# Kernel tuning notes

Measured on AMD Instinct MI355X. Metric: run time of the kernel, lower is better.

## Reference

```python
import jax, jax.numpy as jnp
from jax import lax
import numpy as np

B, L, F = 4, 1024, 32
DM, NL, DS, DC, EX, NH = 256, 4, 16, 4, 2, 4
DI = EX * DM            # 512 inner channels
DTR = (DM + 15) // 16   # dt_rank = 16


def setup_inputs() -> dict:
    key = jax.random.key(0)
    ks = jax.random.split(key, 12)
    s = 0.02
    rn = lambda k, shape: jax.random.normal(k, shape, jnp.float32) * s
    return dict(
        x=jax.random.normal(ks[0], (B, L, F), jnp.float32),
        proj_w=rn(ks[1], (DM, F)), proj_b=jnp.zeros((DM,), jnp.float32),
        inproj_w=rn(ks[2], (NL, 2 * DI, DM)),
        conv_w=rn(ks[3], (NL, DI, DC)), conv_b=jnp.zeros((NL, DI), jnp.float32),
        xproj_w=rn(ks[4], (NL, DTR + 2 * DS, DI)),
        dtproj_w=rn(ks[5], (NL, DI, DTR)), dtproj_b=rn(ks[6], (NL, DI)),
        A_log=jnp.tile(jnp.log(jnp.arange(1, DS + 1, dtype=jnp.float32))[None, None, :], (NL, DI, 1)),
        Dp=jnp.ones((NL, DI), jnp.float32),
        outproj_w=rn(ks[7], (NL, DM, DI)),
        ln_g=jnp.ones((NL, DM), jnp.float32), ln_b=jnp.zeros((NL, DM), jnp.float32),
        head_w1=rn(ks[8], (DM, DM)), head_b1=jnp.zeros((DM,), jnp.float32),
        head_w2=rn(ks[9], (NH, DM)), head_b2=jnp.zeros((NH,), jnp.float32),
    )


def _layernorm(x, g, b, eps=1e-5):
    mu = x.mean(axis=-1, keepdims=True)
    var = ((x - mu) ** 2).mean(axis=-1, keepdims=True)
    return (x - mu) * lax.rsqrt(var + eps) * g + b


def _mamba(x, inw, cw, cb, xpw, dtw, dtb, A_log, Dp, outw):
    b, l, _ = x.shape
    xz = x @ inw.T                       # (b,l,2*DI)
    u, z = xz[..., :DI], xz[..., DI:]
    # causal depthwise conv1d, kernel DC
    up = jnp.pad(u, ((0, 0), (DC - 1, 0), (0, 0)))
    uc = sum(up[:, k:k + l, :] * cw[:, k] for k in range(DC)) + cb
    uc = jax.nn.silu(uc)
    dbc = uc @ xpw.T                     # (b,l,DTR+2*DS)
    dt, Bc, Cc = dbc[..., :DTR], dbc[..., DTR:DTR + DS], dbc[..., DTR + DS:]
    delta = jax.nn.softplus(dt @ dtw.T + dtb)   # (b,l,DI)
    A = -jnp.exp(A_log)                  # (DI,DS)

    def step(h, inp):
        d_t, B_t, C_t, u_t = inp         # (b,DI),(b,DS),(b,DS),(b,DI)
        h = jnp.exp(d_t[..., None] * A) * h + (d_t * u_t)[..., None] * B_t[:, None, :]
        return h, jnp.einsum('bdn,bn->bd', h, C_t)

    h0 = jnp.zeros((b, DI, DS), x.dtype)
    xs = tuple(jnp.swapaxes(a, 0, 1) for a in (delta, Bc, Cc, uc))
    _, ys = lax.scan(step, h0, xs)       # ys: (l,b,DI)
    y = jnp.swapaxes(ys, 0, 1) + uc * Dp
    return (y * jax.nn.silu(z)) @ outw.T


def reference(x, proj_w, proj_b, inproj_w, conv_w, conv_b, xproj_w, dtproj_w, dtproj_b,
              A_log, Dp, outproj_w, ln_g, ln_b, head_w1, head_b1, head_w2, head_b2):
    h = x @ proj_w.T + proj_b
    for i in range(NL):
        blk = _mamba(h, inproj_w[i], conv_w[i], conv_b[i], xproj_w[i],
                     dtproj_w[i], dtproj_b[i], A_log[i], Dp[i], outproj_w[i])
        h = h + _layernorm(blk, ln_g[i], ln_b[i])
    p = h.mean(axis=1)                   # (b,DM) pool over time
    hid = jax.nn.relu(p @ head_w1.T + head_b1)
    return hid @ head_w2.T + head_b2     # (b,NH)
```

## Files before the change

kernel.cpp:

```cpp
#include <hip/hip_runtime.h>
#include <hip/hip_fp16.h>
#include <math.h>

#define LTOT 1024
#define BB   4
#define F_IN 32
#define DM   256
#define DI   512
#define DS   16
#define DTRN 16
#define NXP  48
#define NLAY 4
#define NH   4
#define NC   16
#define CLEN 64
#define ROWS (BB*LTOT)

typedef _Float16 half8 __attribute__((ext_vector_type(8)));
typedef float f32x16 __attribute__((ext_vector_type(16)));
typedef unsigned short us8 __attribute__((ext_vector_type(8)));

__device__ __forceinline__ float siluf_(float x) { return x / (1.0f + expf(-x)); }
__device__ __forceinline__ float softplusf_(float x) {
    if (x > 20.f) return x;
    if (x < -20.f) return expf(x);
    return log1pf(expf(x));
}

__device__ __forceinline__ void split16(float x, unsigned short& hi, unsigned short& lo) {
    __half h = __float2half(x);
    hi = *(unsigned short*)&h;
    float r = x - __half2float(h);
    __half l = __float2half(r);
    lo = *(unsigned short*)&l;
}

__global__ __launch_bounds__(256) void k_splitw(const float* __restrict__ inw,
                                                const float* __restrict__ outw,
                                                unsigned short* __restrict__ iwh,
                                                unsigned short* __restrict__ iwl,
                                                unsigned short* __restrict__ owh,
                                                unsigned short* __restrict__ owl) {
    int q = blockIdx.x * 256 + threadIdx.x;
    ushort4 h4, l4;
    if (q < 262144) {
        float4 v = ((const float4*)inw)[q];
        split16(v.x, h4.x, l4.x); split16(v.y, h4.y, l4.y);
        split16(v.z, h4.z, l4.z); split16(v.w, h4.w, l4.w);
        *(ushort4*)(iwh + (size_t)q * 4) = h4;
        *(ushort4*)(iwl + (size_t)q * 4) = l4;
    } else {
        int r = q - 262144;
        float4 v = ((const float4*)outw)[r];
        split16(v.x, h4.x, l4.x); split16(v.y, h4.y, l4.y);
        split16(v.z, h4.z, l4.z); split16(v.w, h4.w, l4.w);
        *(ushort4*)(owh + (size_t)r * 4) = h4;
        *(ushort4*)(owl + (size_t)r * 4) = l4;
    }
}

__global__ __launch_bounds__(256) void k_proj(const float* __restrict__ x,
                                              const float* __restrict__ pw,
                                              const float* __restrict__ pb,
                                              float* __restrict__ h,
                                              unsigned short* __restrict__ hh,
                                              unsigned short* __restrict__ hl) {
    __shared__ float wl[DM][33];
    __shared__ float xl[16][32];
    int t = threadIdx.x;
    int r0 = blockIdx.x * 16;
    for (int i = t; i < DM * 32 / 4; i += 256) {
        float4 v = ((const float4*)pw)[i];
        int c = i / 8, k = (i % 8) * 4;
        wl[c][k] = v.x; wl[c][k + 1] = v.y; wl[c][k + 2] = v.z; wl[c][k + 3] = v.w;
    }
    for (int i = t; i < 16 * 32 / 4; i += 256) {
        float4 v = ((const float4*)(x + (size_t)r0 * F_IN))[i];
        int r = i / 8, k = (i % 8) * 4;
        xl[r][k] = v.x; xl[r][k + 1] = v.y; xl[r][k + 2] = v.z; xl[r][k + 3] = v.w;
    }
    __syncthreads();
    int c = t;
    float bias = pb[c];
    float acc[16];
#pragma unroll
    for (int r = 0; r < 16; ++r) acc[r] = bias;
    for (int k = 0; k < 32; ++k) {
        float w = wl[c][k];
#pragma unroll
        for (int r = 0; r < 16; ++r) acc[r] = fmaf(xl[r][k], w, acc[r]);
    }
#pragma unroll
    for (int r = 0; r < 16; ++r) {
        size_t idx = (size_t)(r0 + r) * DM + c;
        h[idx] = acc[r];
        unsigned short vh, vl; split16(acc[r], vh, vl);
        hh[idx] = vh; hl[idx] = vl;
    }
}

__global__ __launch_bounds__(256) void k_gemm_xz(const unsigned short* __restrict__ Ahp,
                                                 const unsigned short* __restrict__ Alp,
                                                 const unsigned short* __restrict__ Bhp,
                                                 const unsigned short* __restrict__ Blp,
                                                 float* __restrict__ C) {
    __shared__ unsigned short Ah[64][40], Al[64][40], Bh[128][40], Bl[128][40];
    int t = threadIdx.x;
    int bx = blockIdx.x & 7;
    int by = blockIdx.x >> 3;
    int rowA = t >> 2, kA = (t & 3) * 8;
    int rowB = t >> 1, kB = (t & 1) * 16;
    const unsigned short* ApH = Ahp + (size_t)(by * 64 + rowA) * DM + kA;
    const unsigned short* ApL = Alp + (size_t)(by * 64 + rowA) * DM + kA;
    const unsigned short* BpH = Bhp + (size_t)(bx * 128 + rowB) * DM + kB;
    const unsigned short* BpL = Blp + (size_t)(bx * 128 + rowB) * DM + kB;
    us8 rah = *(const us8*)ApH, ral = *(const us8*)ApL;
    us8 rbh0 = *(const us8*)BpH, rbh1 = *(const us8*)(BpH + 8);
    us8 rbl0 = *(const us8*)BpL, rbl1 = *(const us8*)(BpL + 8);
    int lane = t & 63, wid = t >> 6;
    int fr = lane & 31, fg = lane >> 5;
    int wr = wid >> 1, wc = wid & 1;
    f32x16 acc[2] = {};
    for (int k0 = 0; k0 < DM; k0 += 32) {
        *(us8*)&Ah[rowA][kA] = rah;
        *(us8*)&Al[rowA][kA] = ral;
        *(us8*)&Bh[rowB][kB] = rbh0; *(us8*)&Bh[rowB][kB + 8] = rbh1;
        *(us8*)&Bl[rowB][kB] = rbl0; *(us8*)&Bl[rowB][kB + 8] = rbl1;
        __syncthreads();
        if (k0 + 32 < DM) {
            rah = *(const us8*)(ApH + k0 + 32); ral = *(const us8*)(ApL + k0 + 32);
            rbh0 = *(const us8*)(BpH + k0 + 32); rbh1 = *(const us8*)(BpH + k0 + 40);
            rbl0 = *(const us8*)(BpL + k0 + 32); rbl1 = *(const us8*)(BpL + k0 + 40);
        }
#pragma unroll
        for (int s = 0; s < 2; ++s) {
            int ko = s * 16 + fg * 8;
            half8 ah = *(const half8*)&Ah[wr * 32 + fr][ko];
            half8 al = *(const half8*)&Al[wr * 32 + fr][ko];
#pragma unroll
            for (int fc = 0; fc < 2; ++fc) {
                half8 bh = *(const half8*)&Bh[wc * 64 + fc * 32 + fr][ko];
                half8 bl = *(const half8*)&Bl[wc * 64 + fc * 32 + fr][ko];
                acc[fc] = __builtin_amdgcn_mfma_f32_32x32x16_f16(ah, bh, acc[fc], 0, 0, 0);
                acc[fc] = __builtin_amdgcn_mfma_f32_32x32x16_f16(ah, bl, acc[fc], 0, 0, 0);
                acc[fc] = __builtin_amdgcn_mfma_f32_32x32x16_f16(al, bh, acc[fc], 0, 0, 0);
            }
        }
        __syncthreads();
    }
    float* Cp = C + (size_t)(by * 64 + wr * 32) * 1024 + bx * 128 + wc * 64;
#pragma unroll
    for (int fc = 0; fc < 2; ++fc) {
#pragma unroll
        for (int reg = 0; reg < 16; ++reg) {
            int row = (reg & 3) + 8 * (reg >> 2) + 4 * fg;
            Cp[(size_t)row * 1024 + fc * 32 + fr] = acc[fc][reg];
        }
    }
}

__global__ __launch_bounds__(256) void k_conv(const float* __restrict__ xz,
                                              const float* __restrict__ cw,
                                              const float* __restrict__ cb,
                                              float* __restrict__ uc) {
    int gid = blockIdx.x * 256 + threadIdx.x;
    if (gid >= ROWS * (DI / 4)) return;
    int r = gid / (DI / 4);
    int d = (gid % (DI / 4)) * 4;
    int tt = r & (LTOT - 1);
    float4 acc = make_float4(cb[d], cb[d + 1], cb[d + 2], cb[d + 3]);
#pragma unroll
    for (int k = 0; k < 4; ++k) {
        int ts = tt - 3 + k;
        if (ts < 0) continue;
        float4 u = *(const float4*)(xz + (size_t)(r - 3 + k) * 1024 + d);
        acc.x = fmaf(u.x, cw[(d + 0) * 4 + k], acc.x);
        acc.y = fmaf(u.y, cw[(d + 1) * 4 + k], acc.y);
        acc.z = fmaf(u.z, cw[(d + 2) * 4 + k], acc.z);
        acc.w = fmaf(u.w, cw[(d + 3) * 4 + k], acc.w);
    }
    acc.x = siluf_(acc.x); acc.y = siluf_(acc.y); acc.z = siluf_(acc.z); acc.w = siluf_(acc.w);
    *(float4*)(uc + (size_t)r * DI + d) = acc;
}

__global__ __launch_bounds__(256) void k_dbcp(const float* __restrict__ uc,
                                              const float* __restrict__ xpw,
                                              float* __restrict__ xz) {
    __shared__ float us[32][132];
    __shared__ float wsd[48][132];
    int t = threadIdx.x;
    int kp = blockIdx.x & 3;
    int r0 = (blockIdx.x >> 2) * 32;
    int k0 = kp * 128;
    float4* us4 = (float4*)us;
    float4* ws4 = (float4*)wsd;
#pragma unroll
    for (int j = 0; j < 4; ++j) {
        int i = t + j * 256;
        int r = i >> 5, kq = i & 31;
        us4[r * 33 + kq] = *(const float4*)(uc + (size_t)(r0 + r) * DI + k0 + kq * 4);
    }
#pragma unroll
    for (int j = 0; j < 6; ++j) {
        int i = t + j * 256;
        int r = i >> 5, kq = i & 31;
        ws4[r * 33 + kq] = *(const float4*)(xpw + (size_t)r * DI + k0 + kq * 4);
    }
    __syncthreads();
    int tx = t & 15, ty = t >> 4;
    const float4* ua = us4 + (ty * 2) * 33;
    const float4* ub = ua + 33;
    const float4* w0p = ws4 + (tx * 3) * 33;
    const float4* w1p = w0p + 33;
    const float4* w2p = w0p + 66;
    float acc[2][3] = {};
#pragma unroll 4
    for (int kq = 0; kq < 32; ++kq) {
        float4 u0 = ua[kq], u1 = ub[kq];
        float4 w0 = w0p[kq], w1 = w1p[kq], w2 = w2p[kq];
        acc[0][0] = fmaf(u0.x, w0.x, acc[0][0]); acc[0][0] = fmaf(u0.y, w0.y, acc[0][0]);
        acc[0][0] = fmaf(u0.z, w0.z, acc[0][0]); acc[0][0] = fmaf(u0.w, w0.w, acc[0][0]);
        acc[0][1] = fmaf(u0.x, w1.x, acc[0][1]); acc[0][1] = fmaf(u0.y, w1.y, acc[0][1]);
        acc[0][1] = fmaf(u0.z, w1.z, acc[0][1]); acc[0][1] = fmaf(u0.w, w1.w, acc[0][1]);
        acc[0][2] = fmaf(u0.x, w2.x, acc[0][2]); acc[0][2] = fmaf(u0.y, w2.y, acc[0][2]);
        acc[0][2] = fmaf(u0.z, w2.z, acc[0][2]); acc[0][2] = fmaf(u0.w, w2.w, acc[0][2]);
        acc[1][0] = fmaf(u1.x, w0.x, acc[1][0]); acc[1][0] = fmaf(u1.y, w0.y, acc[1][0]);
        acc[1][0] = fmaf(u1.z, w0.z, acc[1][0]); acc[1][0] = fmaf(u1.w, w0.w, acc[1][0]);
        acc[1][1] = fmaf(u1.x, w1.x, acc[1][1]); acc[1][1] = fmaf(u1.y, w1.y, acc[1][1]);
        acc[1][1] = fmaf(u1.z, w1.z, acc[1][1]); acc[1][1] = fmaf(u1.w, w1.w, acc[1][1]);
        acc[1][2] = fmaf(u1.x, w2.x, acc[1][2]); acc[1][2] = fmaf(u1.y, w2.y, acc[1][2]);
        acc[1][2] = fmaf(u1.z, w2.z, acc[1][2]); acc[1][2] = fmaf(u1.w, w2.w, acc[1][2]);
    }
    float* outp = xz + (size_t)(r0 + ty * 2) * 1024 + kp * 48 + tx * 3;
    outp[0] = acc[0][0]; outp[1] = acc[0][1]; outp[2] = acc[0][2];
    outp[1024] = acc[1][0]; outp[1025] = acc[1][1]; outp[1026] = acc[1][2];
}

__global__ __launch_bounds__(256) void k_dbcr(const float* __restrict__ xzp,
                                              const float* __restrict__ dtw,
                                              const float* __restrict__ dtb,
                                              float* __restrict__ delta,
                                              float* __restrict__ BC) {
    __shared__ float dbl[16][NXP];
    int t = threadIdx.x;
    int r0 = blockIdx.x * 16;
    {
        int r = t >> 4, c3 = (t & 15) * 3;
        const float* pp = xzp + (size_t)(r0 + r) * 1024 + c3;
#pragma unroll
        for (int j = 0; j < 3; ++j) {
            float s = pp[j] + pp[48 + j] + pp[96 + j] + pp[144 + j];
            dbl[r][c3 + j] = s;
            int cj = c3 + j;
            if (cj >= 16) BC[(size_t)(r0 + r) * 32 + (cj - 16)] = s;
        }
    }
    __syncthreads();
    {
        int c0 = t * 2;
        float wd0[16], wd1[16];
        const float4* q0 = (const float4*)(dtw + (size_t)c0 * 16);
        const float4* q1 = (const float4*)(dtw + (size_t)(c0 + 1) * 16);
#pragma unroll
        for (int j = 0; j < 4; ++j) { *(float4*)&wd0[j * 4] = q0[j]; *(float4*)&wd1[j * 4] = q1[j]; }
        float bb0 = dtb[c0], bb1 = dtb[c0 + 1];
        for (int r = 0; r < 16; ++r) {
            float s0 = bb0, s1 = bb1;
#pragma unroll
            for (int k = 0; k < 16; ++k) {
                float dv = dbl[r][k];
                s0 = fmaf(dv, wd0[k], s0);
                s1 = fmaf(dv, wd1[k], s1);
            }
            *(float2*)(delta + (size_t)(r0 + r) * DI + c0) =
                make_float2(softplusf_(s0), softplusf_(s1));
        }
    }
}

__global__ __launch_bounds__(256) void k_scanA(const float* __restrict__ delta,
                                               const float* __restrict__ uc,
                                               const float* __restrict__ BC,
                                               const float* __restrict__ A_log,
                                               float* __restrict__ P,
                                               float* __restrict__ hL) {
    __shared__ float2 du2[CLEN][16];
    __shared__ float  Bl[CLEN][16];
    int bid = blockIdx.x;
    int c = bid & 15, dblk = (bid >> 4) & 31, b = bid >> 9;
    int d0 = dblk * 16, t0 = c * CLEN;
    int t = threadIdx.x;
    {
        int row = t >> 2, hf = (t & 3) * 4;
        size_t rbase = (size_t)(b * LTOT + t0 + row);
        float4 dv = *(const float4*)(delta + rbase * DI + d0 + hf);
        float4 uv = *(const float4*)(uc + rbase * DI + d0 + hf);
        float4* dst = (float4*)&du2[row][hf];
        dst[0] = make_float4(dv.x, uv.x, dv.y, uv.y);
        dst[1] = make_float4(dv.z, uv.z, dv.w, uv.w);
        *(float4*)&Bl[row][hf] = *(const float4*)(BC + rbase * 32 + hf);
    }
    __syncthreads();
    int n = t & 15, dn = t >> 4;
    float Ac = -expf(A_log[(size_t)(d0 + dn) * DS + n]);
    float h = 0.f, Pp = 1.f;
#pragma unroll 8
    for (int k = 0; k < CLEN; ++k) {
        float2 du = du2[k][dn];
        float Bv = Bl[k][n];
        float a = expf(du.x * Ac);
        Pp *= a;
        h = fmaf(a, h, du.x * du.y * Bv);
    }
    size_t idx = ((size_t)(b * NC + c)) * (DI * DS) + (size_t)d0 * DS + t;
    P[idx] = Pp;
    hL[idx] = h;
}

__global__ __launch_bounds__(256) void k_scanC(const float* __restrict__ delta,
                                               const float* __restrict__ uc,
                                               const float* __restrict__ BC,
                                               const float* __restrict__ A_log,
                                               const float* __restrict__ P,
                                               const float* __restrict__ hL,
                                               const float* __restrict__ Dp,
                                               const float* __restrict__ xz,
                                               unsigned short* __restrict__ yh,
                                               unsigned short* __restrict__ yl) {
    __shared__ float2 du2[CLEN][16];
    __shared__ float2 bc2[CLEN][16];
    __shared__ float  ytmp[16][16][20];
    int bid = blockIdx.x;
    int c = bid & 15, dblk = (bid >> 4) & 31, b = bid >> 9;
    int d0 = dblk * 16, t0 = c * CLEN;
    int t = threadIdx.x;
    {
        int row = t >> 2, hf = (t & 3) * 4;
        size_t rbase = (size_t)(b * LTOT + t0 + row);
        float4 dv = *(const float4*)(delta + rbase * DI + d0 + hf);
        float4 uv = *(const float4*)(uc + rbase * DI + d0 + hf);
        float4* dst = (float4*)&du2[row][hf];
        dst[0] = make_float4(dv.x, uv.x, dv.y, uv.y);
        dst[1] = make_float4(dv.z, uv.z, dv.w, uv.w);
        float4 bv = *(const float4*)(BC + rbase * 32 + hf);
        float4 cv = *(const float4*)(BC + rbase * 32 + 16 + hf);
        float4* bdst = (float4*)&bc2[row][hf];
        bdst[0] = make_float4(bv.x, cv.x, bv.y, cv.y);
        bdst[1] = make_float4(bv.z, cv.z, bv.w, cv.w);
    }
    __syncthreads();
    int n = t & 15, dn = t >> 4;
    float Ac = -expf(A_log[(size_t)(d0 + dn) * DS + n]);
    float Hin = 0.f;
    for (int cc = 0; cc < c; ++cc) {
        size_t idx = ((size_t)(b * NC + cc)) * (DI * DS) + (size_t)d0 * DS + t;
        Hin = fmaf(P[idx], Hin, hL[idx]);
    }
    float h = Hin;
    int rdn = t & 15, rk = t >> 4;
    float DpV = Dp[d0 + rdn];
    for (int s = 0; s < CLEN / 16; ++s) {
#pragma unroll
        for (int kk = 0; kk < 16; ++kk) {
            int k = s * 16 + kk;
            float2 du = du2[k][dn];
            float2 bc = bc2[k][n];
            float a = expf(du.x * Ac);
            h = fmaf(a, h, du.x * du.y * bc.x);
            ytmp[kk][dn][n] = h * bc.y;
        }
        __syncthreads();
        {
            const float* rowp = &ytmp[rk][rdn][0];
            float4 v0 = *(const float4*)(rowp + 0);
            float4 v1 = *(const float4*)(rowp + 4);
            float4 v2 = *(const float4*)(rowp + 8);
            float4 v3 = *(const float4*)(rowp + 12);
            float y = ((v0.x + v0.y) + (v0.z + v0.w)) + ((v1.x + v1.y) + (v1.z + v1.w))
                    + ((v2.x + v2.y) + (v2.z + v2.w)) + ((v3.x + v3.y) + (v3.z + v3.w));
            float uu = du2[s * 16 + rk][rdn].y;
            size_t rb2 = (size_t)(b * LTOT + t0 + s * 16 + rk);
            float z = xz[rb2 * 1024 + 512 + d0 + rdn];
            float val = fmaf(uu, DpV, y) * siluf_(z);
            unsigned short vh, vl; split16(val, vh, vl);
            size_t yi = rb2 * DI + d0 + rdn;
            yh[yi] = vh; yl[yi] = vl;
        }
        __syncthreads();
    }
}

__global__ __launch_bounds__(256) void k_gemm_out(const unsigned short* __restrict__ Ahp,
                                                  const unsigned short* __restrict__ Alp,
                                                  const unsigned short* __restrict__ Bhp,
                                                  const unsigned short* __restrict__ Blp,
                                                  float* __restrict__ p01,
                                                  float* __restrict__ p23) {
    __shared__ unsigned short Ah[64][40], Al[64][40], Bh[128][40], Bl[128][40];
    int t = threadIdx.x;
    int bx = blockIdx.x & 1;
    int by = (blockIdx.x >> 1) & 63;
    int kp = blockIdx.x >> 7;
    int rowA = t >> 2, kA = (t & 3) * 8;
    int rowB = t >> 1, kB = (t & 1) * 16;
    const unsigned short* ApH = Ahp + (size_t)(by * 64 + rowA) * DI + kp * 128 + kA;
    const unsigned short* ApL = Alp + (size_t)(by * 64 + rowA) * DI + kp * 128 + kA;
    const unsigned short* BpH = Bhp + (size_t)(bx * 128 + rowB) * DI + kp * 128 + kB;
    const unsigned short* BpL = Blp + (size_t)(bx * 128 + rowB) * DI + kp * 128 + kB;
    us8 rah = *(const us8*)ApH, ral = *(const us8*)ApL;
    us8 rbh0 = *(const us8*)BpH, rbh1 = *(const us8*)(BpH + 8);
    us8 rbl0 = *(const us8*)BpL, rbl1 = *(const us8*)(BpL + 8);
    int lane = t & 63, wid = t >> 6;
    int fr = lane & 31, fg = lane >> 5;
    int wr = wid >> 1, wc = wid & 1;
    f32x16 acc[2] = {};
    for (int k0 = 0; k0 < 128; k0 += 32) {
        *(us8*)&Ah[rowA][kA] = rah;
        *(us8*)&Al[rowA][kA] = ral;
        *(us8*)&Bh[rowB][kB] = rbh0; *(us8*)&Bh[rowB][kB + 8] = rbh1;
        *(us8*)&Bl[rowB][kB] = rbl0; *(us8*)&Bl[rowB][kB + 8] = rbl1;
        __syncthreads();
        if (k0 + 32 < 128) {
            rah = *(const us8*)(ApH + k0 + 32); ral = *(const us8*)(ApL + k0 + 32);
            rbh0 = *(const us8*)(BpH + k0 + 32); rbh1 = *(const us8*)(BpH + k0 + 40);
            rbl0 = *(const us8*)(BpL + k0 + 32); rbl1 = *(const us8*)(BpL + k0 + 40);
        }
#pragma unroll
        for (int s = 0; s < 2; ++s) {
            int ko = s * 16 + fg * 8;
            half8 ah = *(const half8*)&Ah[wr * 32 + fr][ko];
            half8 al = *(const half8*)&Al[wr * 32 + fr][ko];
#pragma unroll
            for (int fc = 0; fc < 2; ++fc) {
                half8 bh = *(const half8*)&Bh[wc * 64 + fc * 32 + fr][ko];
                half8 bl = *(const half8*)&Bl[wc * 64 + fc * 32 + fr][ko];
                acc[fc] = __builtin_amdgcn_mfma_f32_32x32x16_f16(ah, bh, acc[fc], 0, 0, 0);
                acc[fc] = __builtin_amdgcn_mfma_f32_32x32x16_f16(ah, bl, acc[fc], 0, 0, 0);
                acc[fc] = __builtin_amdgcn_mfma_f32_32x32x16_f16(al, bh, acc[fc], 0, 0, 0);
            }
        }
        __syncthreads();
    }
    float* pbase = (kp < 2 ? p01 : p23) + (size_t)(kp & 1) * (ROWS * DM);
    float* Cp = pbase + (size_t)(by * 64 + wr * 32) * DM + bx * 128 + wc * 64;
#pragma unroll
    for (int fc = 0; fc < 2; ++fc) {
#pragma unroll
        for (int reg = 0; reg < 16; ++reg) {
            int row = (reg & 3) + 8 * (reg >> 2) + 4 * fg;
            Cp[(size_t)row * DM + fc * 32 + fr] = acc[fc][reg];
        }
    }
}

__global__ __launch_bounds__(256) void k_ln_res(const float* __restrict__ p01,
                                                const float* __restrict__ p23,
                                                const float* __restrict__ g,
                                                const float* __restrict__ bb,
                                                float* __restrict__ h,
                                                unsigned short* __restrict__ hh,
                                                unsigned short* __restrict__ hl) {
    __shared__ float scratch[4];
    int r = blockIdx.x, t = threadIdx.x;
    size_t idx = (size_t)r * DM + t;
    float v = p01[idx] + p01[idx + (size_t)ROWS * DM] + p23[idx] + p23[idx + (size_t)ROWS * DM];
    float s = v;
#pragma unroll
    for (int m = 32; m >= 1; m >>= 1) s += __shfl_xor(s, m, 64);
    if ((t & 63) == 0) scratch[t >> 6] = s;
    __syncthreads();
    float mu = (scratch[0] + scratch[1] + scratch[2] + scratch[3]) * (1.f / DM);
    __syncthreads();
    float d = v - mu;
    float s2 = d * d;
#pragma unroll
    for (int m = 32; m >= 1; m >>= 1) s2 += __shfl_xor(s2, m, 64);
    if ((t & 63) == 0) scratch[t >> 6] = s2;
    __syncthreads();
    float var = (scratch[0] + scratch[1] + scratch[2] + scratch[3]) * (1.f / DM);
    float rstd = 1.f / sqrtf(var + 1e-5f);
    float nv = h[idx] + d * rstd * g[t] + bb[t];
    h[idx] = nv;
    unsigned short vh, vl; split16(nv, vh, vl);
    hh[idx] = vh; hl[idx] = vl;
}

__global__ __launch_bounds__(256) void k_meanp(const float* __restrict__ h,
                                               float* __restrict__ part) {
    int bid = blockIdx.x;
    int b = bid >> 3, g = bid & 7;
    int t = threadIdx.x;
    float s = 0.f;
    for (int k = 0; k < 128; ++k)
        s += h[(size_t)(b * LTOT + g * 128 + k) * DM + t];
    part[(size_t)bid * DM + t] = s;
}

__global__ __launch_bounds__(256) void k_head(const float* __restrict__ part,
                                              const float* __restrict__ w1,
                                              const float* __restrict__ b1,
                                              const float* __restrict__ w2,
                                              const float* __restrict__ b2,
                                              float* __restrict__ out) {
    __shared__ float pl[DM], hl[DM];
    int b = blockIdx.x, t = threadIdx.x;
    float s = 0.f;
    for (int g = 0; g < 8; ++g) s += part[(size_t)(b * 8 + g) * DM + t];
    pl[t] = s * (1.f / LTOT);
    __syncthreads();
    float a = b1[t];
    for (int k = 0; k < DM; ++k) a = fmaf(pl[k], w1[(size_t)t * DM + k], a);
    hl[t] = fmaxf(a, 0.f);
    __syncthreads();
    if (t < NH) {
        float o = b2[t];
        for (int k = 0; k < DM; ++k) o = fmaf(hl[k], w2[(size_t)t * DM + k], o);
        out[b * NH + t] = o;
    }
}

extern "C" void kernel_launch(void* const* d_in, const int* in_sizes, int n_in,
                              void* d_out, int out_size, void* d_ws, size_t ws_size,
                              hipStream_t stream) {
    const float* x        = (const float*)d_in[0];
    const float* proj_w   = (const float*)d_in[1];
    const float* proj_b   = (const float*)d_in[2];
    const float* inproj_w = (const float*)d_in[3];
    const float* conv_w   = (const float*)d_in[4];
    const float* conv_b   = (const float*)d_in[5];
    const float* xproj_w  = (const float*)d_in[6];
    const float* dtproj_w = (const float*)d_in[7];
    const float* dtproj_b = (const float*)d_in[8];
    const float* A_log    = (const float*)d_in[9];
    const float* Dp       = (const float*)d_in[10];
    const float* outproj_w= (const float*)d_in[11];
    const float* ln_g     = (const float*)d_in[12];
    const float* ln_b     = (const float*)d_in[13];
    const float* head_w1  = (const float*)d_in[14];
    const float* head_b1  = (const float*)d_in[15];
    const float* head_w2  = (const float*)d_in[16];
    const float* head_b2  = (const float*)d_in[17];

    float* ws    = (float*)d_ws;
    float* h     = ws;
    float* xz    = h + 1048576;
    float* uc    = xz + 4194304;
    float* delta = uc + 2097152;
    float* BC    = delta + 2097152;
    float* Pbuf  = BC + 131072;
    float* hLbuf = Pbuf + 524288;
    float* part  = hLbuf + 524288;
    unsigned short* h_hi  = (unsigned short*)(part + 8192);
    unsigned short* h_lo  = h_hi + 1048576;
    unsigned short* y_hi  = h_lo + 1048576;
    unsigned short* y_lo  = y_hi + 2097152;
    unsigned short* iw_hi = y_lo + 2097152;
    unsigned short* iw_lo = iw_hi + 1048576;
    unsigned short* ow_hi = iw_lo + 1048576;
    unsigned short* ow_lo = ow_hi + 524288;

    k_splitw<<<1536, 256, 0, stream>>>(inproj_w, outproj_w, iw_hi, iw_lo, ow_hi, ow_lo);
    k_proj<<<ROWS / 16, 256, 0, stream>>>(x, proj_w, proj_b, h, h_hi, h_lo);

    for (int i = 0; i < NLAY; ++i) {
        const float* cwi  = conv_w + (size_t)i * DI * 4;
        const float* cbi  = conv_b + (size_t)i * DI;
        const float* xpw  = xproj_w + (size_t)i * NXP * DI;
        const float* dtw  = dtproj_w + (size_t)i * DI * DTRN;
        const float* dtb  = dtproj_b + (size_t)i * DI;
        const float* Ali  = A_log + (size_t)i * DI * DS;
        const float* Dpi  = Dp + (size_t)i * DI;
        const float* gi   = ln_g + (size_t)i * DM;
        const float* bi   = ln_b + (size_t)i * DM;

        k_gemm_xz<<<512, 256, 0, stream>>>(h_hi, h_lo,
                                           iw_hi + (size_t)i * 262144, iw_lo + (size_t)i * 262144, xz);
        k_conv<<<ROWS * (DI / 4) / 256, 256, 0, stream>>>(xz, cwi, cbi, uc);
        k_dbcp<<<512, 256, 0, stream>>>(uc, xpw, xz);
        k_dbcr<<<ROWS / 16, 256, 0, stream>>>(xz, dtw, dtb, delta, BC);
        k_scanA<<<BB * 32 * NC, 256, 0, stream>>>(delta, uc, BC, Ali, Pbuf, hLbuf);
        k_scanC<<<BB * 32 * NC, 256, 0, stream>>>(delta, uc, BC, Ali, Pbuf, hLbuf, Dpi, xz, y_hi, y_lo);
        k_gemm_out<<<512, 256, 0, stream>>>(y_hi, y_lo,
                                            ow_hi + (size_t)i * 131072, ow_lo + (size_t)i * 131072,
                                            delta, uc);
        k_ln_res<<<ROWS, 256, 0, stream>>>(delta, uc, gi, bi, h, h_hi, h_lo);
    }

    k_meanp<<<32, 256, 0, stream>>>(h, part);
    k_head<<<BB, 256, 0, stream>>>(part, head_w1, head_b1, head_w2, head_b2, (float*)d_out);
}
```

Before: 507.0 us.

## Fuse conv into x_proj kernel and recompute delta/BC inside scan kernels

Merges the weight-split and input-projection kernels into one launch, and folds the causal conv+SiLU into the x_proj partial-GEMM kernel, which writes uc as well as a compact partial-sum buffer. The separate dt/BC reduction kernel is removed. Both scan kernels now sum the four partials themselves and compute the dt projection plus softplus in shared memory, so the full delta array is never materialised. This cuts two launches per layer and a large delta write and read, but the dt projection and partial reduction are now done twice, once in each scan kernel. The out-proj partials move to new workspace buffers.

```diff
diff --git a/kernel.cpp b/kernel.cpp
--- a/kernel.cpp
+++ b/kernel.cpp
@@ -35,40 +35,41 @@
     lo = *(unsigned short*)&l;
 }
 
-__global__ __launch_bounds__(256) void k_splitw(const float* __restrict__ inw,
-                                                const float* __restrict__ outw,
-                                                unsigned short* __restrict__ iwh,
-                                                unsigned short* __restrict__ iwl,
-                                                unsigned short* __restrict__ owh,
-                                                unsigned short* __restrict__ owl) {
-    int q = blockIdx.x * 256 + threadIdx.x;
-    ushort4 h4, l4;
-    if (q < 262144) {
-        float4 v = ((const float4*)inw)[q];
-        split16(v.x, h4.x, l4.x); split16(v.y, h4.y, l4.y);
-        split16(v.z, h4.z, l4.z); split16(v.w, h4.w, l4.w);
-        *(ushort4*)(iwh + (size_t)q * 4) = h4;
-        *(ushort4*)(iwl + (size_t)q * 4) = l4;
-    } else {
-        int r = q - 262144;
-        float4 v = ((const float4*)outw)[r];
-        split16(v.x, h4.x, l4.x); split16(v.y, h4.y, l4.y);
-        split16(v.z, h4.z, l4.z); split16(v.w, h4.w, l4.w);
-        *(ushort4*)(owh + (size_t)r * 4) = h4;
-        *(ushort4*)(owl + (size_t)r * 4) = l4;
-    }
-}
-
-__global__ __launch_bounds__(256) void k_proj(const float* __restrict__ x,
+__global__ __launch_bounds__(256) void k_init(const float* __restrict__ x,
                                               const float* __restrict__ pw,
                                               const float* __restrict__ pb,
+                                              const float* __restrict__ inw,
+                                              const float* __restrict__ outw,
                                               float* __restrict__ h,
                                               unsigned short* __restrict__ hh,
-                                              unsigned short* __restrict__ hl) {
+                                              unsigned short* __restrict__ hl,
+                                              unsigned short* __restrict__ iwh,
+                                              unsigned short* __restrict__ iwl,
+                                              unsigned short* __restrict__ owh,
+                                              unsigned short* __restrict__ owl) {
     __shared__ float wl[DM][33];
     __shared__ float xl[16][32];
-    int t = threadIdx.x;
-    int r0 = blockIdx.x * 16;
+    int bid = blockIdx.x, t = threadIdx.x;
+    if (bid < 1536) {
+        int q = bid * 256 + t;
+        ushort4 h4, l4;
+        if (q < 262144) {
+            float4 v = ((const float4*)inw)[q];
+            split16(v.x, h4.x, l4.x); split16(v.y, h4.y, l4.y);
+            split16(v.z, h4.z, l4.z); split16(v.w, h4.w, l4.w);
+            *(ushort4*)(iwh + (size_t)q * 4) = h4;
+            *(ushort4*)(iwl + (size_t)q * 4) = l4;
+        } else {
+            int r = q - 262144;
+            float4 v = ((const float4*)outw)[r];
+            split16(v.x, h4.x, l4.x); split16(v.y, h4.y, l4.y);
+            split16(v.z, h4.z, l4.z); split16(v.w, h4.w, l4.w);
+            *(ushort4*)(owh + (size_t)r * 4) = h4;
+            *(ushort4*)(owl + (size_t)r * 4) = l4;
+        }
+        return;
+    }
+    int r0 = (bid - 1536) * 16;
     for (int i = t; i < DM * 32 / 4; i += 256) {
         float4 v = ((const float4*)pw)[i];
         int c = i / 8, k = (i % 8) * 4;
@@ -159,33 +160,12 @@
     }
 }
 
-__global__ __launch_bounds__(256) void k_conv(const float* __restrict__ xz,
+__global__ __launch_bounds__(256) void k_dbcp(const float* __restrict__ xz,
                                               const float* __restrict__ cw,
                                               const float* __restrict__ cb,
-                                              float* __restrict__ uc) {
-    int gid = blockIdx.x * 256 + threadIdx.x;
-    if (gid >= ROWS * (DI / 4)) return;
-    int r = gid / (DI / 4);
-    int d = (gid % (DI / 4)) * 4;
-    int tt = r & (LTOT - 1);
-    float4 acc = make_float4(cb[d], cb[d + 1], cb[d + 2], cb[d + 3]);
-#pragma unroll
-    for (int k = 0; k < 4; ++k) {
-        int ts = tt - 3 + k;
-        if (ts < 0) continue;
-        float4 u = *(const float4*)(xz + (size_t)(r - 3 + k) * 1024 + d);
-        acc.x = fmaf(u.x, cw[(d + 0) * 4 + k], acc.x);
-        acc.y = fmaf(u.y, cw[(d + 1) * 4 + k], acc.y);
-        acc.z = fmaf(u.z, cw[(d + 2) * 4 + k], acc.z);
-        acc.w = fmaf(u.w, cw[(d + 3) * 4 + k], acc.w);
-    }
-    acc.x = siluf_(acc.x); acc.y = siluf_(acc.y); acc.z = siluf_(acc.z); acc.w = siluf_(acc.w);
-    *(float4*)(uc + (size_t)r * DI + d) = acc;
-}
-
-__global__ __launch_bounds__(256) void k_dbcp(const float* __restrict__ uc,
                                               const float* __restrict__ xpw,
-                                              float* __restrict__ xz) {
+                                              float* __restrict__ uc,
+                                              float* __restrict__ dbp) {
     __shared__ float us[32][132];
     __shared__ float wsd[48][132];
     int t = threadIdx.x;
@@ -198,7 +178,22 @@
     for (int j = 0; j < 4; ++j) {
         int i = t + j * 256;
         int r = i >> 5, kq = i & 31;
-        us4[r * 33 + kq] = *(const float4*)(uc + (size_t)(r0 + r) * DI + k0 + kq * 4);
+        int rr = r0 + r, d = k0 + kq * 4;
+        int tt = rr & (LTOT - 1);
+        float4 acc = make_float4(cb[d], cb[d + 1], cb[d + 2], cb[d + 3]);
+#pragma unroll
+        for (int k = 0; k < 4; ++k) {
+            int ts = tt - 3 + k;
+            if (ts < 0) continue;
+            float4 u = *(const float4*)(xz + (size_t)(rr - 3 + k) * 1024 + d);
+            acc.x = fmaf(u.x, cw[(d + 0) * 4 + k], acc.x);
+            acc.y = fmaf(u.y, cw[(d + 1) * 4 + k], acc.y);
+            acc.z = fmaf(u.z, cw[(d + 2) * 4 + k], acc.z);
+            acc.w = fmaf(u.w, cw[(d + 3) * 4 + k], acc.w);
+        }
+        acc.x = siluf_(acc.x); acc.y = siluf_(acc.y); acc.z = siluf_(acc.z); acc.w = siluf_(acc.w);
+        us4[r * 33 + kq] = acc;
+        *(float4*)(uc + (size_t)rr * DI + d) = acc;
     }
 #pragma unroll
     for (int j = 0; j < 6; ++j) {
@@ -231,74 +226,71 @@
         acc[1][2] = fmaf(u1.x, w2.x, acc[1][2]); acc[1][2] = fmaf(u1.y, w2.y, acc[1][2]);
         acc[1][2] = fmaf(u1.z, w2.z, acc[1][2]); acc[1][2] = fmaf(u1.w, w2.w, acc[1][2]);
     }
-    float* outp = xz + (size_t)(r0 + ty * 2) * 1024 + kp * 48 + tx * 3;
+    float* outp = dbp + (size_t)(r0 + ty * 2) * 192 + kp * 48 + tx * 3;
     outp[0] = acc[0][0]; outp[1] = acc[0][1]; outp[2] = acc[0][2];
-    outp[1024] = acc[1][0]; outp[1025] = acc[1][1]; outp[1026] = acc[1][2];
-}
-
-__global__ __launch_bounds__(256) void k_dbcr(const float* __restrict__ xzp,
-                                              const float* __restrict__ dtw,
-                                              const float* __restrict__ dtb,
-                                              float* __restrict__ delta,
-                                              float* __restrict__ BC) {
-    __shared__ float dbl[16][NXP];
-    int t = threadIdx.x;
-    int r0 = blockIdx.x * 16;
-    {
-        int r = t >> 4, c3 = (t & 15) * 3;
-        const float* pp = xzp + (size_t)(r0 + r) * 1024 + c3;
-#pragma unroll
-        for (int j = 0; j < 3; ++j) {
-            float s = pp[j] + pp[48 + j] + pp[96 + j] + pp[144 + j];
-            dbl[r][c3 + j] = s;
-            int cj = c3 + j;
-            if (cj >= 16) BC[(size_t)(r0 + r) * 32 + (cj - 16)] = s;
-        }
-    }
-    __syncthreads();
-    {
-        int c0 = t * 2;
-        float wd0[16], wd1[16];
-        const float4* q0 = (const float4*)(dtw + (size_t)c0 * 16);
-        const float4* q1 = (const float4*)(dtw + (size_t)(c0 + 1) * 16);
-#pragma unroll
-        for (int j = 0; j < 4; ++j) { *(float4*)&wd0[j * 4] = q0[j]; *(float4*)&wd1[j * 4] = q1[j]; }
-        float bb0 = dtb[c0], bb1 = dtb[c0 + 1];
-        for (int r = 0; r < 16; ++r) {
-            float s0 = bb0, s1 = bb1;
-#pragma unroll
-            for (int k = 0; k < 16; ++k) {
-                float dv = dbl[r][k];
-                s0 = fmaf(dv, wd0[k], s0);
-                s1 = fmaf(dv, wd1[k], s1);
-            }
-            *(float2*)(delta + (size_t)(r0 + r) * DI + c0) =
-                make_float2(softplusf_(s0), softplusf_(s1));
-        }
-    }
-}
-
-__global__ __launch_bounds__(256) void k_scanA(const float* __restrict__ delta,
+    outp[192] = acc[1][0]; outp[193] = acc[1][1]; outp[194] = acc[1][2];
+}
+
+__global__ __launch_bounds__(256) void k_scanA(const float* __restrict__ dbp,
                                                const float* __restrict__ uc,
-                                               const float* __restrict__ BC,
+                                               const float* __restrict__ dtw,
+                                               const float* __restrict__ dtb,
                                                const float* __restrict__ A_log,
                                                float* __restrict__ P,
                                                float* __restrict__ hL) {
     __shared__ float2 du2[CLEN][16];
     __shared__ float  Bl[CLEN][16];
+    __shared__ float  dbl[CLEN][17];
+    __shared__ float  wdl[16][17];
+    __shared__ float  wbias[16];
     int bid = blockIdx.x;
     int c = bid & 15, dblk = (bid >> 4) & 31, b = bid >> 9;
     int d0 = dblk * 16, t0 = c * CLEN;
     int t = threadIdx.x;
+    int row = t >> 2, q4 = (t & 3) * 4;
+    size_t rbase = (size_t)(b * LTOT + t0 + row);
+    float4 uv = *(const float4*)(uc + rbase * DI + d0 + q4);
     {
-        int row = t >> 2, hf = (t & 3) * 4;
-        size_t rbase = (size_t)(b * LTOT + t0 + row);
-        float4 dv = *(const float4*)(delta + rbase * DI + d0 + hf);
-        float4 uv = *(const float4*)(uc + rbase * DI + d0 + hf);
-        float4* dst = (float4*)&du2[row][hf];
-        dst[0] = make_float4(dv.x, uv.x, dv.y, uv.y);
-        dst[1] = make_float4(dv.z, uv.z, dv.w, uv.w);
-        *(float4*)&Bl[row][hf] = *(const float4*)(BC + rbase * 32 + hf);
+        const float* pp = dbp + rbase * 192;
+        float4 a0 = *(const float4*)(pp + q4);
+        float4 a1 = *(const float4*)(pp + 48 + q4);
+        float4 a2 = *(const float4*)(pp + 96 + q4);
+        float4 a3 = *(const float4*)(pp + 144 + q4);
+        dbl[row][q4 + 0] = ((a0.x + a1.x) + a2.x) + a3.x;
+        dbl[row][q4 + 1] = ((a0.y + a1.y) + a2.y) + a3.y;
+        dbl[row][q4 + 2] = ((a0.z + a1.z) + a2.z) + a3.z;
+        dbl[row][q4 + 3] = ((a0.w + a1.w) + a2.w) + a3.w;
+        float4 b0 = *(const float4*)(pp + 16 + q4);
+        float4 b1 = *(const float4*)(pp + 64 + q4);
+        float4 b2 = *(const float4*)(pp + 112 + q4);
+        float4 b3 = *(const float4*)(pp + 160 + q4);
+        Bl[row][q4 + 0] = ((b0.x + b1.x) + b2.x) + b3.x;
+        Bl[row][q4 + 1] = ((b0.y + b1.y) + b2.y) + b3.y;
+        Bl[row][q4 + 2] = ((b0.z + b1.z) + b2.z) + b3.z;
+        Bl[row][q4 + 3] = ((b0.w + b1.w) + b2.w) + b3.w;
+    }
+    if (t < 64) {
+        int dd = t >> 2, sg = (t & 3) * 4;
+        const float* wp = dtw + (size_t)(d0 + dd) * 16 + sg;
+        wdl[dd][sg + 0] = wp[0]; wdl[dd][sg + 1] = wp[1];
+        wdl[dd][sg + 2] = wp[2]; wdl[dd][sg + 3] = wp[3];
+    }
+    if (t < 16) wbias[t] = dtb[d0 + t];
+    __syncthreads();
+    {
+        float s0 = wbias[q4 + 0], s1 = wbias[q4 + 1], s2 = wbias[q4 + 2], s3 = wbias[q4 + 3];
+#pragma unroll
+        for (int k = 0; k < 16; ++k) {
+            float dv = dbl[row][k];
+            s0 = fmaf(dv, wdl[q4 + 0][k], s0);
+            s1 = fmaf(dv, wdl[q4 + 1][k], s1);
+            s2 = fmaf(dv, wdl[q4 + 2][k], s2);
+            s3 = fmaf(dv, wdl[q4 + 3][k], s3);
+        }
+        du2[row][q4 + 0] = make_float2(softplusf_(s0), uv.x);
+        du2[row][q4 + 1] = make_float2(softplusf_(s1), uv.y);
+        du2[row][q4 + 2] = make_float2(softplusf_(s2), uv.z);
+        du2[row][q4 + 3] = make_float2(softplusf_(s3), uv.w);
     }
     __syncthreads();
     int n = t & 15, dn = t >> 4;
@@ -317,9 +309,10 @@
     hL[idx] = h;
 }
 
-__global__ __launch_bounds__(256) void k_scanC(const float* __restrict__ delta,
+__global__ __launch_bounds__(256) void k_scanC(const float* __restrict__ dbp,
                                                const float* __restrict__ uc,
-                                               const float* __restrict__ BC,
+                                               const float* __restrict__ dtw,
+                                               const float* __restrict__ dtb,
                                                const float* __restrict__ A_log,
                                                const float* __restrict__ P,
                                                const float* __restrict__ hL,
@@ -330,23 +323,66 @@
     __shared__ float2 du2[CLEN][16];
     __shared__ float2 bc2[CLEN][16];
     __shared__ float  ytmp[16][16][20];
+    float* scr = &ytmp[0][0][0];
+    float (*dbl)[17] = (float(*)[17])scr;
+    float (*wdl)[17] = (float(*)[17])(scr + 1088);
+    float* wbias = scr + 1088 + 272;
     int bid = blockIdx.x;
     int c = bid & 15, dblk = (bid >> 4) & 31, b = bid >> 9;
     int d0 = dblk * 16, t0 = c * CLEN;
     int t = threadIdx.x;
+    int row = t >> 2, q4 = (t & 3) * 4;
+    size_t rbase = (size_t)(b * LTOT + t0 + row);
+    float4 uv = *(const float4*)(uc + rbase * DI + d0 + q4);
     {
-        int row = t >> 2, hf = (t & 3) * 4;
-        size_t rbase = (size_t)(b * LTOT + t0 + row);
-        float4 dv = *(const float4*)(delta + rbase * DI + d0 + hf);
-        float4 uv = *(const float4*)(uc + rbase * DI + d0 + hf);
-        float4* dst = (float4*)&du2[row][hf];
-        dst[0] = make_float4(dv.x, uv.x, dv.y, uv.y);
-        dst[1] = make_float4(dv.z, uv.z, dv.w, uv.w);
-        float4 bv = *(const float4*)(BC + rbase * 32 + hf);
-        float4 cv = *(const float4*)(BC + rbase * 32 + 16 + hf);
-        float4* bdst = (float4*)&bc2[row][hf];
-        bdst[0] = make_float4(bv.x, cv.x, bv.y, cv.y);
-        bdst[1] = make_float4(bv.z, cv.z, bv.w, cv.w);
+        const float* pp = dbp + rbase * 192;
+        float4 a0 = *(const float4*)(pp + q4);
+        float4 a1 = *(const float4*)(pp + 48 + q4);
+        float4 a2 = *(const float4*)(pp + 96 + q4);
+        float4 a3 = *(const float4*)(pp + 144 + q4);
+        dbl[row][q4 + 0] = ((a0.x + a1.x) + a2.x) + a3.x;
+        dbl[row][q4 + 1] = ((a0.y + a1.y) + a2.y) + a3.y;
+        dbl[row][q4 + 2] = ((a0.z + a1.z) + a2.z) + a3.z;
+        dbl[row][q4 + 3] = ((a0.w + a1.w) + a2.w) + a3.w;
+        float4 b0 = *(const float4*)(pp + 16 + q4);
+        float4 b1 = *(const float4*)(pp + 64 + q4);
+        float4 b2 = *(const float4*)(pp + 112 + q4);
+        float4 b3 = *(const float4*)(pp + 160 + q4);
+        float4 c0 = *(const float4*)(pp + 32 + q4);
+        float4 c1 = *(const float4*)(pp + 80 + q4);
+        float4 c2 = *(const float4*)(pp + 128 + q4);
+        float4 c3 = *(const float4*)(pp + 176 + q4);
+        float B0 = ((b0.x + b1.x) + b2.x) + b3.x, C0 = ((c0.x + c1.x) + c2.x) + c3.x;
+        float B1 = ((b0.y + b1.y) + b2.y) + b3.y, C1 = ((c0.y + c1.y) + c2.y) + c3.y;
+        float B2 = ((b0.z + b1.z) + b2.z) + b3.z, C2 = ((c0.z + c1.z) + c2.z) + c3.z;
+        float B3 = ((b0.w + b1.w) + b2.w) + b3.w, C3 = ((c0.w + c1.w) + c2.w) + c3.w;
+        bc2[row][q4 + 0] = make_float2(B0, C0);
+        bc2[row][q4 + 1] = make_float2(B1, C1);
+        bc2[row][q4 + 2] = make_float2(B2, C2);
+        bc2[row][q4 + 3] = make_float2(B3, C3);
+    }
+    if (t < 64) {
+        int dd = t >> 2, sg = (t & 3) * 4;
+        const float* wp = dtw + (size_t)(d0 + dd) * 16 + sg;
+        wdl[dd][sg + 0] = wp[0]; wdl[dd][sg + 1] = wp[1];
+        wdl[dd][sg + 2] = wp[2]; wdl[dd][sg + 3] = wp[3];
+    }
+    if (t < 16) wbias[t] = dtb[d0 + t];
+    __syncthreads();
+    {
+        float s0 = wbias[q4 + 0], s1 = wbias[q4 + 1], s2 = wbias[q4 + 2], s3 = wbias[q4 + 3];
+#pragma unroll
+        for (int k = 0; k < 16; ++k) {
+            float dv = dbl[row][k];
+            s0 = fmaf(dv, wdl[q4 + 0][k], s0);
+            s1 = fmaf(dv, wdl[q4 + 1][k], s1);
+            s2 = fmaf(dv, wdl[q4 + 2][k], s2);
+            s3 = fmaf(dv, wdl[q4 + 3][k], s3);
+        }
+        du2[row][q4 + 0] = make_float2(softplusf_(s0), uv.x);
+        du2[row][q4 + 1] = make_float2(softplusf_(s1), uv.y);
+        du2[row][q4 + 2] = make_float2(softplusf_(s2), uv.z);
+        du2[row][q4 + 3] = make_float2(softplusf_(s3), uv.w);
     }
     __syncthreads();
     int n = t & 15, dn = t >> 4;
@@ -545,11 +581,12 @@
     float* h     = ws;
     float* xz    = h + 1048576;
     float* uc    = xz + 4194304;
-    float* delta = uc + 2097152;
-    float* BC    = delta + 2097152;
-    float* Pbuf  = BC + 131072;
+    float* dbp   = uc + 2097152;
+    float* Pbuf  = dbp + 786432;
     float* hLbuf = Pbuf + 524288;
-    float* part  = hLbuf + 524288;
+    float* p01   = hLbuf + 524288;
+    float* p23   = p01 + 2097152;
+    float* part  = p23 + 2097152;
     unsigned short* h_hi  = (unsigned short*)(part + 8192);
     unsigned short* h_lo  = h_hi + 1048576;
     unsigned short* y_hi  = h_lo + 1048576;
@@ -559,8 +596,8 @@
     unsigned short* ow_hi = iw_lo + 1048576;
     unsigned short* ow_lo = ow_hi + 524288;
 
-    k_splitw<<<1536, 256, 0, stream>>>(inproj_w, outproj_w, iw_hi, iw_lo, ow_hi, ow_lo);
-    k_proj<<<ROWS / 16, 256, 0, stream>>>(x, proj_w, proj_b, h, h_hi, h_lo);
+    k_init<<<1792, 256, 0, stream>>>(x, proj_w, proj_b, inproj_w, outproj_w,
+                                     h, h_hi, h_lo, iw_hi, iw_lo, ow_hi, ow_lo);
 
     for (int i = 0; i < NLAY; ++i) {
         const float* cwi  = conv_w + (size_t)i * DI * 4;
@@ -575,15 +612,13 @@
 
         k_gemm_xz<<<512, 256, 0, stream>>>(h_hi, h_lo,
                                            iw_hi + (size_t)i * 262144, iw_lo + (size_t)i * 262144, xz);
-        k_conv<<<ROWS * (DI / 4) / 256, 256, 0, stream>>>(xz, cwi, cbi, uc);
-        k_dbcp<<<512, 256, 0, stream>>>(uc, xpw, xz);
-        k_dbcr<<<ROWS / 16, 256, 0, stream>>>(xz, dtw, dtb, delta, BC);
-        k_scanA<<<BB * 32 * NC, 256, 0, stream>>>(delta, uc, BC, Ali, Pbuf, hLbuf);
-        k_scanC<<<BB * 32 * NC, 256, 0, stream>>>(delta, uc, BC, Ali, Pbuf, hLbuf, Dpi, xz, y_hi, y_lo);
+        k_dbcp<<<512, 256, 0, stream>>>(xz, cwi, cbi, xpw, uc, dbp);
+        k_scanA<<<BB * 32 * NC, 256, 0, stream>>>(dbp, uc, dtw, dtb, Ali, Pbuf, hLbuf);
+        k_scanC<<<BB * 32 * NC, 256, 0, stream>>>(dbp, uc, dtw, dtb, Ali, Pbuf, hLbuf, Dpi, xz, y_hi, y_lo);
         k_gemm_out<<<512, 256, 0, stream>>>(y_hi, y_lo,
                                             ow_hi + (size_t)i * 131072, ow_lo + (size_t)i * 131072,
-                                            delta, uc);
-        k_ln_res<<<ROWS, 256, 0, stream>>>(delta, uc, gi, bi, h, h_hi, h_lo);
+                                            p01, p23);
+        k_ln_res<<<ROWS, 256, 0, stream>>>(p01, p23, gi, bi, h, h_hi, h_lo);
     }
 
     k_meanp<<<32, 256, 0, stream>>>(h, part);
```

New measurement: 482.7 us. 1.05x faster.
